# Performance work log

Measured on AMD Instinct MI355X. Metric: run time of the kernel, lower is better.

The kernel has to match this reference:

```python
import jax, jax.numpy as jnp
import numpy as np


def setup_inputs() -> dict:
    key = jax.random.key(0)
    k1, k2 = jax.random.split(key)
    B, C, H, W = 8, 64, 128, 256
    left_feature = jax.random.normal(k1, (B, C, H, W), dtype=jnp.float32)
    right_feature = jax.random.normal(k2, (B, C, H, W), dtype=jnp.float32)
    return {
        "left_feature": left_feature,
        "right_feature": right_feature,
        "max_disp": 64,
    }


def reference(left_feature, right_feature, max_disp):
    # Stereo correlation cost volume (norm=False branch):
    #   volume[b, d, h, w] = mean_c( left[b,c,h,w] * right[b,c,h,w-d] )  for w >= d
    #   volume[b, d, h, w] = 0                                           for w <  d
    b, c, h, w = left_feature.shape

    def corr_at_disp(d):
        # left[:, :, :, d:] * right[:, :, :, :w-d], mean over channel dim
        prod = left_feature[:, :, :, d:] * right_feature[:, :, :, : w - d]
        cv = jnp.mean(prod, axis=1)  # (b, h, w-d)
        # left-pad along width with zeros for invalid disparities
        return jnp.pad(cv, ((0, 0), (0, 0), (d, 0)))

    # max_disp is a static Python int; loop over disparity hyperparameter is static.
    volume = jnp.stack([corr_at_disp(d) for d in range(max_disp)], axis=1)
    return volume  # (b, max_disp, h, w)
```

## Files before the change

### kernel.cpp

```cpp
#include <hip/hip_runtime.h>

typedef _Float16 half8 __attribute__((ext_vector_type(8)));
typedef float floatx4 __attribute__((ext_vector_type(4)));

#define BB 8
#define CC 64
#define HH 128
#define WW 256
#define DD 64

__global__ __launch_bounds__(512, 4)
void corr_volume_mfma(const float* __restrict__ left,
                      const float* __restrict__ right,
                      float* __restrict__ out) {
    __shared__ _Float16 Lb[256 * 64];
    __shared__ _Float16 Rb[320 * 64];

    const int tid  = threadIdx.x;
    const int lane = tid & 63;
    const int wv   = tid >> 6;
    const int bh   = blockIdx.x;
    const int b    = bh >> 7;
    const int h    = bh & 127;

    const size_t chanStride = (size_t)HH * WW;
    const size_t rowBase    = (size_t)b * CC * chanStride + (size_t)h * WW;

    const int sw = lane * 4;
    const int cg = wv;

    const float* lp = left  + rowBase + (size_t)(cg * 8) * chanStride + sw;
    const float* rp = right + rowBase + (size_t)(cg * 8) * chanStride + sw;

    float4 lv[8], rv[8];
    #pragma unroll
    for (int cc = 0; cc < 8; ++cc) {
        lv[cc] = *(const float4*)(lp + (size_t)cc * chanStride);
        rv[cc] = *(const float4*)(rp + (size_t)cc * chanStride);
    }

    {
        half8 z = {0, 0, 0, 0, 0, 0, 0, 0};
        *(half8*)&Rb[tid * 8] = z;
    }

    const float* lf = (const float*)lv;
    const float* rf = (const float*)rv;
    #pragma unroll
    for (int s = 0; s < 4; ++s) {
        const int w   = sw + s;
        const int col = (cg ^ (w & 7)) * 8;
        half8 lh, rh;
        #pragma unroll
        for (int cc = 0; cc < 8; ++cc) {
            lh[cc] = (_Float16)lf[cc * 4 + s];
            rh[cc] = (_Float16)rf[cc * 4 + s];
        }
        *(half8*)&Lb[w * 64 + col]        = lh;
        *(half8*)&Rb[(w + 64) * 64 + col] = rh;
    }
    __syncthreads();

    const int n     = lane & 15;
    const int q     = lane >> 4;
    const int wbase = wv * 32;

    floatx4 acc[2][5];
    #pragma unroll
    for (int t = 0; t < 2; ++t)
        #pragma unroll
        for (int u = 0; u < 5; ++u)
            #pragma unroll
            for (int r = 0; r < 4; ++r)
                acc[t][u][r] = 0.0f;

    #pragma unroll
    for (int kk = 0; kk < 2; ++kk) {
        const int col = ((kk * 4 + q) ^ (n & 7)) * 8;
        half8 bfrag[2], afrag[6];
        #pragma unroll
        for (int t = 0; t < 2; ++t)
            bfrag[t] = *(const half8*)&Lb[(wbase + t * 16 + n) * 64 + col];
        #pragma unroll
        for (int a = 0; a < 6; ++a)
            afrag[a] = *(const half8*)&Rb[(wbase + a * 16 + n) * 64 + col];
        #pragma unroll
        for (int t = 0; t < 2; ++t)
            #pragma unroll
            for (int u = 0; u < 5; ++u)
                acc[t][u] = __builtin_amdgcn_mfma_f32_16x16x32_f16(
                    afrag[t + u], bfrag[t], acc[t][u], 0, 0, 0);
    }

    const float scale = 1.0f / 64.0f;
    #pragma unroll
    for (int t = 0; t < 2; ++t) {
        const int w = wbase + t * 16 + n;
        #pragma unroll
        for (int u = 0; u < 5; ++u) {
            #pragma unroll
            for (int r = 0; r < 4; ++r) {
                const int d = 64 - 16 * u + n - (q * 4 + r);
                if (d >= 0 && d < DD) {
                    out[(((size_t)b * DD + d) * HH + h) * WW + w] =
                        acc[t][u][r] * scale;
                }
            }
        }
    }
}

extern "C" void kernel_launch(void* const* d_in, const int* in_sizes, int n_in,
                              void* d_out, int out_size, void* d_ws, size_t ws_size,
                              hipStream_t stream) {
    const float* left  = (const float*)d_in[0];
    const float* right = (const float*)d_in[1];
    float* out = (float*)d_out;

    dim3 grid(BB * HH);
    dim3 block(512);
    corr_volume_mfma<<<grid, block, 0, stream>>>(left, right, out);
}
```

Baseline: 189.3 us.

## Make blocks persistent over four rows and prefetch the next row's inputs

The grid shrinks from one block per (b,h) row to 256 blocks, and each block loops over 4 rows. While it computes MFMA on the current row, it issues global loads for the next row into registers, overlapping memory latency with compute and output stores. The cost is higher register pressure: launch bounds drop to 2 blocks per SM, and the smaller grid may leave CUs underused or lower the latency hiding that came from occupancy.

```diff
diff --git a/kernel.cpp b/kernel.cpp
--- a/kernel.cpp
+++ b/kernel.cpp
@@ -8,102 +8,128 @@
 #define HH 128
 #define WW 256
 #define DD 64
+#define NROW 4
+#define GRID 256
 
-__global__ __launch_bounds__(512, 4)
+__global__ __launch_bounds__(512, 2)
 void corr_volume_mfma(const float* __restrict__ left,
                       const float* __restrict__ right,
                       float* __restrict__ out) {
-    __shared__ _Float16 Lb[256 * 64];
-    __shared__ _Float16 Rb[320 * 64];
+    __shared__ alignas(16) _Float16 Lb[256 * 64];
+    __shared__ alignas(16) _Float16 Rb[320 * 64];
 
     const int tid  = threadIdx.x;
     const int lane = tid & 63;
     const int wv   = tid >> 6;
-    const int bh   = blockIdx.x;
-    const int b    = bh >> 7;
-    const int h    = bh & 127;
+    const int sw   = lane * 4;
+    const int cg   = wv;
 
     const size_t chanStride = (size_t)HH * WW;
-    const size_t rowBase    = (size_t)b * CC * chanStride + (size_t)h * WW;
-
-    const int sw = lane * 4;
-    const int cg = wv;
-
-    const float* lp = left  + rowBase + (size_t)(cg * 8) * chanStride + sw;
-    const float* rp = right + rowBase + (size_t)(cg * 8) * chanStride + sw;
-
-    float4 lv[8], rv[8];
-    #pragma unroll
-    for (int cc = 0; cc < 8; ++cc) {
-        lv[cc] = *(const float4*)(lp + (size_t)cc * chanStride);
-        rv[cc] = *(const float4*)(rp + (size_t)cc * chanStride);
-    }
 
     {
         half8 z = {0, 0, 0, 0, 0, 0, 0, 0};
         *(half8*)&Rb[tid * 8] = z;
     }
 
-    const float* lf = (const float*)lv;
-    const float* rf = (const float*)rv;
-    #pragma unroll
-    for (int s = 0; s < 4; ++s) {
-        const int w   = sw + s;
-        const int col = (cg ^ (w & 7)) * 8;
-        half8 lh, rh;
+    float4 lv[8], rv[8];
+
+    {
+        const int bh = blockIdx.x;
+        const size_t rowBase = (size_t)(bh >> 7) * CC * chanStride
+                             + (size_t)(bh & 127) * WW;
+        const float* lp = left  + rowBase + (size_t)(cg * 8) * chanStride + sw;
+        const float* rp = right + rowBase + (size_t)(cg * 8) * chanStride + sw;
         #pragma unroll
-        for (int cc = 0; cc < 8; ++cc) {
-            lh[cc] = (_Float16)lf[cc * 4 + s];
-            rh[cc] = (_Float16)rf[cc * 4 + s];
+        for (int c = 0; c < 8; ++c) {
+            lv[c] = *(const float4*)(lp + (size_t)c * chanStride);
+            rv[c] = *(const float4*)(rp + (size_t)c * chanStride);
         }
-        *(half8*)&Lb[w * 64 + col]        = lh;
-        *(half8*)&Rb[(w + 64) * 64 + col] = rh;
     }
-    __syncthreads();
 
-    const int n     = lane & 15;
-    const int q     = lane >> 4;
+    const int n = lane & 15;
+    const int q = lane >> 4;
     const int wbase = wv * 32;
-
-    floatx4 acc[2][5];
-    #pragma unroll
-    for (int t = 0; t < 2; ++t)
-        #pragma unroll
-        for (int u = 0; u < 5; ++u)
-            #pragma unroll
-            for (int r = 0; r < 4; ++r)
-                acc[t][u][r] = 0.0f;
+    const float scale = 1.0f / 64.0f;
 
     #pragma unroll
-    for (int kk = 0; kk < 2; ++kk) {
-        const int col = ((kk * 4 + q) ^ (n & 7)) * 8;
-        half8 bfrag[2], afrag[6];
-        #pragma unroll
-        for (int t = 0; t < 2; ++t)
-            bfrag[t] = *(const half8*)&Lb[(wbase + t * 16 + n) * 64 + col];
-        #pragma unroll
-        for (int a = 0; a < 6; ++a)
-            afrag[a] = *(const half8*)&Rb[(wbase + a * 16 + n) * 64 + col];
+    for (int k = 0; k < NROW; ++k) {
+        const int bh = blockIdx.x + k * GRID;
+        const int b  = bh >> 7;
+        const int h  = bh & 127;
+
+        __syncthreads();
+
+        {
+            const float* lf = (const float*)lv;
+            const float* rf = (const float*)rv;
+            #pragma unroll
+            for (int s = 0; s < 4; ++s) {
+                const int w   = sw + s;
+                const int col = (cg ^ (w & 7)) * 8;
+                half8 lh, rh;
+                #pragma unroll
+                for (int c = 0; c < 8; ++c) {
+                    lh[c] = (_Float16)lf[c * 4 + s];
+                    rh[c] = (_Float16)rf[c * 4 + s];
+                }
+                *(half8*)&Lb[w * 64 + col]        = lh;
+                *(half8*)&Rb[(w + 64) * 64 + col] = rh;
+            }
+        }
+        __syncthreads();
+
+        if (k + 1 < NROW) {
+            const int bh2 = blockIdx.x + (k + 1) * GRID;
+            const size_t rowBase2 = (size_t)(bh2 >> 7) * CC * chanStride
+                                  + (size_t)(bh2 & 127) * WW;
+            const float* lp = left  + rowBase2 + (size_t)(cg * 8) * chanStride + sw;
+            const float* rp = right + rowBase2 + (size_t)(cg * 8) * chanStride + sw;
+            #pragma unroll
+            for (int c = 0; c < 8; ++c) {
+                lv[c] = *(const float4*)(lp + (size_t)c * chanStride);
+                rv[c] = *(const float4*)(rp + (size_t)c * chanStride);
+            }
+        }
+
+        floatx4 acc[2][5];
         #pragma unroll
         for (int t = 0; t < 2; ++t)
             #pragma unroll
             for (int u = 0; u < 5; ++u)
-                acc[t][u] = __builtin_amdgcn_mfma_f32_16x16x32_f16(
-                    afrag[t + u], bfrag[t], acc[t][u], 0, 0, 0);
-    }
+                #pragma unroll
+                for (int r = 0; r < 4; ++r)
+                    acc[t][u][r] = 0.0f;
 
-    const float scale = 1.0f / 64.0f;
-    #pragma unroll
-    for (int t = 0; t < 2; ++t) {
-        const int w = wbase + t * 16 + n;
         #pragma unroll
-        for (int u = 0; u < 5; ++u) {
+        for (int kk = 0; kk < 2; ++kk) {
+            const int col = ((kk * 4 + q) ^ (n & 7)) * 8;
+            half8 bfrag[2], afrag[6];
             #pragma unroll
-            for (int r = 0; r < 4; ++r) {
-                const int d = 64 - 16 * u + n - (q * 4 + r);
-                if (d >= 0 && d < DD) {
-                    out[(((size_t)b * DD + d) * HH + h) * WW + w] =
-                        acc[t][u][r] * scale;
+            for (int t = 0; t < 2; ++t)
+                bfrag[t] = *(const half8*)&Lb[(wbase + t * 16 + n) * 64 + col];
+            #pragma unroll
+            for (int a = 0; a < 6; ++a)
+                afrag[a] = *(const half8*)&Rb[(wbase + a * 16 + n) * 64 + col];
+            #pragma unroll
+            for (int t = 0; t < 2; ++t)
+                #pragma unroll
+                for (int u = 0; u < 5; ++u)
+                    acc[t][u] = __builtin_amdgcn_mfma_f32_16x16x32_f16(
+                        afrag[t + u], bfrag[t], acc[t][u], 0, 0, 0);
+        }
+
+        #pragma unroll
+        for (int t = 0; t < 2; ++t) {
+            const int w = wbase + t * 16 + n;
+            #pragma unroll
+            for (int u = 0; u < 5; ++u) {
+                #pragma unroll
+                for (int r = 0; r < 4; ++r) {
+                    const int d = 64 - 16 * u + n - (q * 4 + r);
+                    if (d >= 0 && d < DD) {
+                        out[(((size_t)b * DD + d) * HH + h) * WW + w] =
+                            acc[t][u][r] * scale;
+                    }
                 }
             }
         }
@@ -117,7 +143,7 @@
     const float* right = (const float*)d_in[1];
     float* out = (float*)d_out;
 
-    dim3 grid(BB * HH);
+    dim3 grid(GRID);
     dim3 block(512);
     corr_volume_mfma<<<grid, block, 0, stream>>>(left, right, out);
 }
```

Result: no change. 186.7 us (-1.4%).
